# Optimization experiments

Measured on AMD Instinct MI355X. Metric: run time of the kernel, lower is better.

The kernel has to match this reference:

```python
import jax, jax.numpy as jnp
import numpy as np

HEADS = 24
HEAD_DIM = 128
EPS = 1e-6


def _rms_norm(x, w):
    # normalize over last dim (head_dim)
    var = jnp.mean(jnp.square(x), axis=-1, keepdims=True)
    return x * jax.lax.rsqrt(var + EPS) * w


def _rope_interleaved(x, cos, sin):
    # x: [B, S_img, H, D], cos/sin: [S_img, D//2]; non-neox (interleaved) style
    x1 = x[..., 0::2]
    x2 = x[..., 1::2]
    c = cos[None, :, None, :]
    s = sin[None, :, None, :]
    o1 = x1 * c - x2 * s
    o2 = x2 * c + x1 * s
    return jnp.stack([o1, o2], axis=-1).reshape(x.shape)


def setup_inputs() -> dict:
    key = jax.random.key(0)
    ks = jax.random.split(key, 5)
    B, S, D = 2, 2304, HEADS * HEAD_DIM
    S_img = 2048
    return {
        "hidden_states": jax.random.normal(ks[0], (B, S, D), dtype=jnp.float32),
        "w_qkv": jax.random.normal(ks[1], (3 * D, D), dtype=jnp.float32) * 0.02,
        "b_qkv": jax.random.normal(ks[2], (3 * D,), dtype=jnp.float32) * 0.02,
        "wq_norm": jnp.ones((HEAD_DIM,), dtype=jnp.float32),
        "wk_norm": jnp.ones((HEAD_DIM,), dtype=jnp.float32),
        "cos": jax.random.uniform(ks[3], (S_img, HEAD_DIM // 2), dtype=jnp.float32),
        "sin": jax.random.uniform(ks[4], (S_img, HEAD_DIM // 2), dtype=jnp.float32),
        "text_seq_len": 256,
    }


def reference(hidden_states, w_qkv, b_qkv, wq_norm, wk_norm, cos, sin, text_seq_len):
    B, S, D = hidden_states.shape
    T = text_seq_len
    # fused QKV projection
    qkv = hidden_states @ w_qkv.T + b_qkv  # [B, S, 3D]
    q, k, v = jnp.split(qkv, 3, axis=-1)
    q = q.reshape(B, S, HEADS, HEAD_DIM)
    k = k.reshape(B, S, HEADS, HEAD_DIM)
    v = v.reshape(B, S, HEADS, HEAD_DIM)
    # per-head RMSNorm on query/key
    q = _rms_norm(q, wq_norm)
    k = _rms_norm(k, wk_norm)
    # partial RoPE: only non-text (image/video) tokens
    q = jnp.concatenate([q[:, :T], _rope_interleaved(q[:, T:], cos, sin)], axis=1)
    k = jnp.concatenate([k[:, :T], _rope_interleaved(k[:, T:], cos, sin)], axis=1)
    # non-causal attention, scale = 1/sqrt(head_dim)
    scale = 1.0 / np.sqrt(HEAD_DIM).astype(np.float32)
    scores = jnp.einsum("bqhd,bkhd->bhqk", q, k) * scale
    probs = jax.nn.softmax(scores, axis=-1)
    out = jnp.einsum("bhqk,bkhd->bqhd", probs, v)
    return out.reshape(B, S, HEADS * HEAD_DIM)
```

## Files before the change

kernel.cpp:

```cpp
#include <hip/hip_runtime.h>
#include <stdint.h>
#include <stddef.h>

#define HEADS 24
#define HD    128
#define BB    2
#define SS    2304
#define DD    3072
#define NN3   9216
#define MM    4608

typedef unsigned short ushort_t;
typedef __bf16 bf16x8 __attribute__((ext_vector_type(8)));
typedef float  f32x4  __attribute__((ext_vector_type(4)));

union frag_u { bf16x8 f; uint4 v; unsigned d[4]; };

__device__ __forceinline__ unsigned short f2b(float f) {
  unsigned u = __float_as_uint(f);
  return (unsigned short)((u + 0x7fffu + ((u >> 16) & 1u)) >> 16);
}
__device__ __forceinline__ float b2f(unsigned short s) {
  return __uint_as_float(((unsigned)s) << 16);
}
__device__ __forceinline__ unsigned pkbf(float a, float b) {
  unsigned ua = (__float_as_uint(a) + 0x8000u) >> 16;
  unsigned ub = (__float_as_uint(b) + 0x8000u) & 0xffff0000u;
  return ua | ub;
}

__device__ __forceinline__ void gload_lds16(const void* g, void* l) {
#if __has_builtin(__builtin_amdgcn_global_load_lds)
  __builtin_amdgcn_global_load_lds(
      (const __attribute__((address_space(1))) unsigned int*)g,
      (__attribute__((address_space(3))) unsigned int*)l, 16, 0, 0);
#else
  *(uint4*)l = *(const uint4*)g;
#endif
}

__global__ __launch_bounds__(256) void cvt_bf16_kernel(
    const float* __restrict__ src, ushort_t* __restrict__ dst, int n8)
{
  int i = blockIdx.x * 256 + threadIdx.x;
  if (i >= n8) return;
  const float4* s = (const float4*)src + (size_t)i * 2;
  float4 a = s[0], b = s[1];
  union { ushort_t u[8]; uint4 v; } o;
  o.u[0] = f2b(a.x); o.u[1] = f2b(a.y); o.u[2] = f2b(a.z); o.u[3] = f2b(a.w);
  o.u[4] = f2b(b.x); o.u[5] = f2b(b.y); o.u[6] = f2b(b.z); o.u[7] = f2b(b.w);
  ((uint4*)dst)[i] = o.v;
}

#define BM 128
#define BN 128
#define BK 64
__global__ __launch_bounds__(256) void gemm_qkv_kernel(
    const ushort_t* __restrict__ A, const ushort_t* __restrict__ Bw,
    const float* __restrict__ bias, ushort_t* __restrict__ C)
{
  __shared__ ushort_t Al[BM * BK];
  __shared__ ushort_t Bl[BN * BK];
  const int t = threadIdx.x;
  const int w = t >> 6, l = t & 63;
  const int quad = l >> 4, lq = l & 15;
  const int wm = (w >> 1) << 6, wn = (w & 1) << 6;
  const int m0 = blockIdx.y * BM, n0 = blockIdx.x * BN;

  f32x4 acc[4][4] = {};

  for (int kb = 0; kb < DD; kb += BK) {
    __syncthreads();
#pragma unroll
    for (int i = 0; i < 4; ++i) {
      int c = i * 256 + t;
      int r = c >> 3, sub = c & 7;
      int gs = sub ^ (r & 7);
      gload_lds16(A + (size_t)(m0 + r) * DD + kb + gs * 8, (char*)Al + (size_t)c * 16);
      gload_lds16(Bw + (size_t)(n0 + r) * DD + kb + gs * 8, (char*)Bl + (size_t)c * 16);
    }
    __syncthreads();
#pragma unroll
    for (int ks = 0; ks < 2; ++ks) {
      bf16x8 af[4], bfr[4];
#pragma unroll
      for (int i = 0; i < 4; ++i) {
        int r = wm + i * 16 + lq;
        int ph = ((ks << 2) | quad) ^ (r & 7);
        af[i] = *(const bf16x8*)((const char*)Al + r * 128 + ph * 16);
      }
#pragma unroll
      for (int j = 0; j < 4; ++j) {
        int r = wn + j * 16 + lq;
        int ph = ((ks << 2) | quad) ^ (r & 7);
        bfr[j] = *(const bf16x8*)((const char*)Bl + r * 128 + ph * 16);
      }
#pragma unroll
      for (int i = 0; i < 4; ++i)
#pragma unroll
        for (int j = 0; j < 4; ++j)
          acc[i][j] = __builtin_amdgcn_mfma_f32_16x16x32_bf16(af[i], bfr[j], acc[i][j], 0, 0, 0);
    }
  }
#pragma unroll
  for (int j = 0; j < 4; ++j) {
    int n = n0 + wn + j * 16 + lq;
    float bj = bias[n];
#pragma unroll
    for (int i = 0; i < 4; ++i) {
      int mb = m0 + wm + i * 16 + quad * 4;
#pragma unroll
      for (int r = 0; r < 4; ++r)
        C[(size_t)(mb + r) * NN3 + n] = f2b(acc[i][j][r] + bj);
    }
  }
}

__global__ __launch_bounds__(256) void norm_rope_kernel(
    ushort_t* __restrict__ qkv, const float* __restrict__ wq,
    const float* __restrict__ wk, const float* __restrict__ cosb,
    const float* __restrict__ sinb, const int* __restrict__ tptr)
{
  const int T = *tptr;
  const int t = threadIdx.x, w = t >> 6, l = t & 63;
  int task = blockIdx.x * 4 + w;
  int which = task & 1;
  int rest = task >> 1;
  int h = rest % HEADS;
  int sm = rest / HEADS;
  int s = sm % SS;
  size_t base = (size_t)sm * NN3 + which * DD + h * HD + 2 * l;
  unsigned pr = *(const unsigned*)(qkv + base);
  float x1 = b2f((unsigned short)(pr & 0xffffu));
  float x2 = b2f((unsigned short)(pr >> 16));
  float ss = x1 * x1 + x2 * x2;
#pragma unroll
  for (int m = 1; m < 64; m <<= 1) ss += __shfl_xor(ss, m, 64);
  float rr = rsqrtf(ss * (1.0f / 128.0f) + 1e-6f);
  const float* wn = which ? wk : wq;
  float y1 = x1 * rr * wn[2 * l], y2 = x2 * rr * wn[2 * l + 1];
  if (s >= T) {
    float c = cosb[(size_t)(s - T) * 64 + l];
    float sn = sinb[(size_t)(s - T) * 64 + l];
    float o1 = y1 * c - y2 * sn;
    float o2 = y2 * c + y1 * sn;
    y1 = o1; y2 = o2;
  }
  *(unsigned*)(qkv + base) = (unsigned)f2b(y1) | ((unsigned)f2b(y2) << 16);
}

__global__ __launch_bounds__(256) void vtrans_kernel(
    const ushort_t* __restrict__ qkv, ushort_t* __restrict__ vt)
{
  __shared__ ushort_t Tl[HD * 73];
  const int t = threadIdx.x;
  const int st = blockIdx.x;
  const int bh = blockIdx.y;
  const int b = bh / HEADS, h = bh % HEADS;
  const int s0 = st * 64;
  const ushort_t* vsrc = qkv + (size_t)(b * SS) * NN3 + 2 * DD + h * HD;
#pragma unroll
  for (int i = 0; i < 4; ++i) {
    int c = i * 256 + t;
    int s = c >> 4, dc = c & 15;
    uint4 v4 = *(const uint4*)(vsrc + (size_t)(s0 + s) * NN3 + dc * 8);
    union { uint4 v; ushort_t u[8]; } un; un.v = v4;
#pragma unroll
    for (int j = 0; j < 8; ++j) Tl[(dc * 8 + j) * 73 + s] = un.u[j];
  }
  __syncthreads();
  ushort_t* vdst = vt + (size_t)bh * HD * SS;
#pragma unroll
  for (int i = 0; i < 4; ++i) {
    int c = i * 256 + t;
    int d = c >> 3, sc = c & 7;
    union { uint4 v; ushort_t u[8]; } un;
#pragma unroll
    for (int j = 0; j < 8; ++j) un.u[j] = Tl[d * 73 + sc * 8 + j];
    *(uint4*)(vdst + (size_t)d * SS + s0 + sc * 8) = un.v;
  }
}

__global__ __launch_bounds__(256, 2) void attn_kernel(
    const ushort_t* __restrict__ qkv, const ushort_t* __restrict__ vt,
    float* __restrict__ out)
{
  __shared__ char smem[65536];
  const int t = threadIdx.x;
  const int w = t >> 6, l = t & 63, quad = l >> 4, lq = l & 15;
  const int qt = blockIdx.x, bh = blockIdx.y;
  const int b = bh / HEADS, h = bh % HEADS;
  const int q0 = qt * 128;
  const ushort_t* qb = qkv + (size_t)(b * SS) * NN3 + h * HD;
  const ushort_t* Kg = qb + DD;
  const ushort_t* Vg = vt + (size_t)bh * HD * SS;

  frag_u aq[2][4];
#pragma unroll
  for (int m = 0; m < 2; ++m) {
    size_t ro = (size_t)(q0 + w * 32 + m * 16 + lq) * NN3;
#pragma unroll
    for (int kc = 0; kc < 4; ++kc)
      aq[m][kc].v = *(const uint4*)(qb + ro + kc * 32 + quad * 8);
  }

  frag_u ones;
  ones.d[0] = 0x3f803f80u; ones.d[1] = 0x3f803f80u;
  ones.d[2] = 0x3f803f80u; ones.d[3] = 0x3f803f80u;

  f32x4 o[2][8] = {};
  f32x4 lacc[2] = {};
  const float SC2 = 0.1275174315402f;
  const int rb = ((lq >> 2) << 3) | (lq & 3);

  {
#pragma unroll
    for (int i = 0; i < 4; ++i) {
      int n = i * 256 + t;
      int kv = n >> 4, c = n & 15;
      gload_lds16(Kg + (size_t)kv * NN3 + ((c ^ (kv & 15)) << 3), smem + n * 16);
    }
#pragma unroll
    for (int i = 0; i < 4; ++i) {
      int n = i * 256 + t;
      int dr = n >> 3, c = n & 7;
      gload_lds16(Vg + (size_t)dr * SS + ((c ^ (dr & 7)) << 3), smem + 32768 + n * 16);
    }
  }

  for (int kt = 0; kt < 36; ++kt) {
    char* Ksh = smem + (kt & 1) * 16384;
    char* Vsh = smem + 32768 + (kt & 1) * 16384;
    __syncthreads();
    if (kt + 1 < 36) {
      const int kv1 = (kt + 1) * 64;
      char* Kn = smem + ((kt + 1) & 1) * 16384;
      char* Vn = smem + 32768 + ((kt + 1) & 1) * 16384;
#pragma unroll
      for (int i = 0; i < 4; ++i) {
        int n = i * 256 + t;
        int kv = n >> 4, c = n & 15;
        gload_lds16(Kg + (size_t)(kv1 + kv) * NN3 + ((c ^ (kv & 15)) << 3), Kn + n * 16);
      }
#pragma unroll
      for (int i = 0; i < 4; ++i) {
        int n = i * 256 + t;
        int dr = n >> 3, c = n & 7;
        gload_lds16(Vg + (size_t)dr * SS + kv1 + ((c ^ (dr & 7)) << 3), Vn + n * 16);
      }
    }

    f32x4 sv[2][4] = {};
#pragma unroll
    for (int kc = 0; kc < 4; ++kc) {
#pragma unroll
      for (int kvb = 0; kvb < 4; ++kvb) {
        int row = ((kvb & 2) << 4) + ((kvb & 1) << 2) + rb;
        int swz = ((kc << 2) | quad) ^ (row & 15);
        frag_u a; a.v = *(const uint4*)(Ksh + row * 256 + swz * 16);
        sv[0][kvb] = __builtin_amdgcn_mfma_f32_16x16x32_bf16(a.f, aq[0][kc].f, sv[0][kvb], 0, 0, 0);
        sv[1][kvb] = __builtin_amdgcn_mfma_f32_16x16x32_bf16(a.f, aq[1][kc].f, sv[1][kvb], 0, 0, 0);
      }
    }

    uint2 pb[2][4];
#pragma unroll
    for (int m = 0; m < 2; ++m) {
#pragma unroll
      for (int kvb = 0; kvb < 4; ++kvb) {
        float p0 = exp2f(fmaf(sv[m][kvb][0], SC2, -8.0f));
        float p1 = exp2f(fmaf(sv[m][kvb][1], SC2, -8.0f));
        float p2 = exp2f(fmaf(sv[m][kvb][2], SC2, -8.0f));
        float p3 = exp2f(fmaf(sv[m][kvb][3], SC2, -8.0f));
        pb[m][kvb].x = pkbf(p0, p1);
        pb[m][kvb].y = pkbf(p2, p3);
      }
    }

#pragma unroll
    for (int kc2 = 0; kc2 < 2; ++kc2) {
      frag_u pf0, pf1;
      pf0.d[0] = pb[0][kc2 * 2].x;     pf0.d[1] = pb[0][kc2 * 2].y;
      pf0.d[2] = pb[0][kc2 * 2 + 1].x; pf0.d[3] = pb[0][kc2 * 2 + 1].y;
      pf1.d[0] = pb[1][kc2 * 2].x;     pf1.d[1] = pb[1][kc2 * 2].y;
      pf1.d[2] = pb[1][kc2 * 2 + 1].x; pf1.d[3] = pb[1][kc2 * 2 + 1].y;
      lacc[0] = __builtin_amdgcn_mfma_f32_16x16x32_bf16(ones.f, pf0.f, lacc[0], 0, 0, 0);
      lacc[1] = __builtin_amdgcn_mfma_f32_16x16x32_bf16(ones.f, pf1.f, lacc[1], 0, 0, 0);
#pragma unroll
      for (int dt = 0; dt < 8; ++dt) {
        int row = dt * 16 + lq;
        int swz = ((kc2 << 2) | quad) ^ (row & 7);
        frag_u a; a.v = *(const uint4*)(Vsh + row * 128 + swz * 16);
        o[0][dt] = __builtin_amdgcn_mfma_f32_16x16x32_bf16(a.f, pf0.f, o[0][dt], 0, 0, 0);
        o[1][dt] = __builtin_amdgcn_mfma_f32_16x16x32_bf16(a.f, pf1.f, o[1][dt], 0, 0, 0);
      }
    }
  }

  __syncthreads();
#pragma unroll
  for (int mch = 0; mch < 2; ++mch) {
    float inv = 1.0f / lacc[mch][0];
    int row = w * 16 + lq;
#pragma unroll
    for (int dt = 0; dt < 8; ++dt) {
      f32x4 val = o[mch][dt] * inv;
      int swz = ((dt << 2) | quad) ^ (row & 31);
      *(f32x4*)(smem + row * 512 + swz * 16) = val;
    }
    __syncthreads();
#pragma unroll
    for (int i = 0; i < 8; ++i) {
      int n = i * 256 + t;
      int rr = n >> 5, c = n & 31;
      f32x4 v = *(const f32x4*)(smem + rr * 512 + ((c ^ (rr & 31)) << 4));
      int qg = q0 + ((rr >> 4) << 5) + (mch << 4) + (rr & 15);
      *(f32x4*)(out + (size_t)(b * SS + qg) * DD + h * HD + c * 4) = v;
    }
    __syncthreads();
  }
}

extern "C" void kernel_launch(void* const* d_in, const int* in_sizes, int n_in,
                              void* d_out, int out_size, void* d_ws, size_t ws_size,
                              hipStream_t stream)
{
  const float* hs   = (const float*)d_in[0];
  const float* wqkv = (const float*)d_in[1];
  const float* bq   = (const float*)d_in[2];
  const float* wqn  = (const float*)d_in[3];
  const float* wkn  = (const float*)d_in[4];
  const float* cosb = (const float*)d_in[5];
  const float* sinb = (const float*)d_in[6];
  const int*   tseq = (const int*)d_in[7];
  float* out = (float*)d_out;
  char* ws = (char*)d_ws;

  ushort_t* hsb  = (ushort_t*)ws;
  ushort_t* wb   = (ushort_t*)(ws + 28311552);
  ushort_t* qkvb = (ushort_t*)(ws + 28311552 + 56623104);
  ushort_t* vtb  = hsb;

  cvt_bf16_kernel<<<6912, 256, 0, stream>>>(hs, hsb, 1769472);
  cvt_bf16_kernel<<<13824, 256, 0, stream>>>(wqkv, wb, 3538944);
  gemm_qkv_kernel<<<dim3(72, 36), 256, 0, stream>>>(hsb, wb, bq, qkvb);
  norm_rope_kernel<<<55296, 256, 0, stream>>>(qkvb, wqn, wkn, cosb, sinb, tseq);
  vtrans_kernel<<<dim3(36, 48), 256, 0, stream>>>(qkvb, vtb);
  attn_kernel<<<dim3(18, 48), 256, 0, stream>>>(qkvb, vtb, out);
}
```

Baseline: 796.4 us.

## Rewrite QKV GEMM as 256x256 tile, 8-wave, double-buffered pipelined kernel

Replaces the 128x128 single-buffered QKV GEMM with a 256x256-tile, 512-thread kernel. It double-buffers A/B tiles in 128KB LDS and interleaves global-to-LDS prefetch with MFMA quarter-phases using sched barriers, explicit waitcnts and s_setprio. It also swizzles the block order for L2 locality. The goal is to hide global memory latency and raise data reuse per tile. The trade-offs are far fewer blocks (648), heavy register use for 32 accumulators per lane, and fragile hand-scheduled synchronization.

```diff
diff --git a/kernel.cpp b/kernel.cpp
--- a/kernel.cpp
+++ b/kernel.cpp
@@ -39,6 +39,14 @@
 #endif
 }
 
+#define SCB() __builtin_amdgcn_sched_barrier(0)
+
+__device__ __forceinline__ void barx() {
+  asm volatile("" ::: "memory");
+  __builtin_amdgcn_s_barrier();
+  asm volatile("" ::: "memory");
+}
+
 __global__ __launch_bounds__(256) void cvt_bf16_kernel(
     const float* __restrict__ src, ushort_t* __restrict__ dst, int n8)
 {
@@ -52,63 +60,144 @@
   ((uint4*)dst)[i] = o.v;
 }
 
-#define BM 128
-#define BN 128
-#define BK 64
-__global__ __launch_bounds__(256) void gemm_qkv_kernel(
+#define NITER 24
+
+#define STG(Gp, rowbase, kt, ldsoff) do {                                          \
+    gload_lds16((Gp) + (size_t)((rowbase) + sr) * DD + (kt) * 64 + sgk,            \
+                smem + (ldsoff) + t * 16);                                         \
+    gload_lds16((Gp) + (size_t)((rowbase) + 64 + sr) * DD + (kt) * 64 + sgk,       \
+                smem + (ldsoff) + 8192 + t * 16);                                  \
+  } while (0)
+
+#define LOADA(base, mh) do {                                                       \
+    _Pragma("unroll") for (int ii = 0; ii < 4; ++ii) {                             \
+      int rl = (mh) * 64 + ii * 16 + lq;                                           \
+      _Pragma("unroll") for (int ks = 0; ks < 2; ++ks) {                           \
+        int ph = ((ks << 2) | quad) ^ (lq & 7);                                    \
+        af[ii][ks] = *(const bf16x8*)(smem + (base) + rl * 128 + ph * 16);         \
+      }                                                                            \
+    } } while (0)
+
+#define LOADB(base, nh) do {                                                       \
+    _Pragma("unroll") for (int jj = 0; jj < 2; ++jj) {                             \
+      int j = (nh) * 2 + jj;                                                       \
+      int rl = (wni & 1) * 64 + j * 16 + lq;                                       \
+      _Pragma("unroll") for (int ks = 0; ks < 2; ++ks) {                           \
+        int ph = ((ks << 2) | quad) ^ (lq & 7);                                    \
+        bfr[j][ks] = *(const bf16x8*)(smem + (base) + rl * 128 + ph * 16);         \
+      }                                                                            \
+    } } while (0)
+
+#define MFMAQ(mh, nh) do {                                                         \
+    _Pragma("unroll") for (int ii = 0; ii < 4; ++ii)                               \
+      _Pragma("unroll") for (int jj = 0; jj < 2; ++jj)                             \
+        _Pragma("unroll") for (int ks = 0; ks < 2; ++ks)                           \
+          acc[(mh) * 4 + ii][(nh) * 2 + jj] =                                      \
+              __builtin_amdgcn_mfma_f32_16x16x32_bf16(                             \
+                  af[ii][ks], bfr[(nh) * 2 + jj][ks],                              \
+                  acc[(mh) * 4 + ii][(nh) * 2 + jj], 0, 0, 0);                     \
+  } while (0)
+
+#define PH_MID() do {                                                              \
+    SCB(); barx(); SCB();                                                          \
+    asm volatile("s_waitcnt lgkmcnt(0)" ::: "memory");                             \
+    SCB();                                                                         \
+    __builtin_amdgcn_s_setprio(1);                                                 \
+  } while (0)
+
+#define PH_END() do {                                                              \
+    __builtin_amdgcn_s_setprio(0);                                                 \
+    SCB(); barx(); SCB();                                                          \
+  } while (0)
+
+#define PH_END_W(NWAIT) do {                                                       \
+    __builtin_amdgcn_s_setprio(0);                                                 \
+    SCB();                                                                         \
+    asm volatile("s_waitcnt vmcnt(" #NWAIT ")" ::: "memory");                      \
+    SCB(); barx(); SCB();                                                          \
+  } while (0)
+
+#define ONE_ITER(NL, TA) do {                                                      \
+    const int tb_ = (TA) + 1;                                                      \
+                                       \
+    LOADA(aoffA, 0); LOADB(boffA, 0);                                              \
+    STG(A, m0, tb_, 65536);                                                        \
+    PH_MID(); MFMAQ(0, 0); PH_END();                                               \
+                                       \
+    LOADB(boffA, 1);                                                               \
+    STG(A, m0 + 128, tb_, 65536 + 16384);                                          \
+    PH_MID(); MFMAQ(0, 1); PH_END();                                               \
+                                     \
+    LOADA(aoffA, 1);                                                               \
+    if (NL) STG(Bw, n0, (TA) + 2, 32768);                                          \
+    PH_MID(); MFMAQ(1, 1); PH_END();                                               \
+              \
+    if (NL) STG(Bw, n0 + 128, (TA) + 2, 49152);                                    \
+    PH_MID(); MFMAQ(1, 0);                                                         \
+    if (NL) { PH_END_W(4); } else { PH_END_W(0); }                                 \
+                                     \
+    LOADA(65536 + aoffA, 0); LOADB(65536 + boffA, 0);                              \
+    if (NL) STG(A, m0, (TA) + 2, 0);                                               \
+    PH_MID(); MFMAQ(0, 0); PH_END();                                               \
+                                     \
+    LOADB(65536 + boffA, 1);                                                       \
+    if (NL) STG(A, m0 + 128, (TA) + 2, 16384);                                     \
+    PH_MID(); MFMAQ(0, 1); PH_END();                                               \
+                                     \
+    LOADA(65536 + aoffA, 1);                                                       \
+    if (NL) STG(Bw, n0, tb_ + 2, 98304);                                           \
+    PH_MID(); MFMAQ(1, 1); PH_END();                                               \
+            \
+    if (NL) STG(Bw, n0 + 128, tb_ + 2, 114688);                                    \
+    PH_MID(); MFMAQ(1, 0);                                                         \
+    if (NL) { PH_END_W(4); } else { PH_END(); }                                    \
+  } while (0)
+
+__global__ __launch_bounds__(512, 2) void gemm_qkv_kernel(
     const ushort_t* __restrict__ A, const ushort_t* __restrict__ Bw,
     const float* __restrict__ bias, ushort_t* __restrict__ C)
 {
-  __shared__ ushort_t Al[BM * BK];
-  __shared__ ushort_t Bl[BN * BK];
+  __shared__ char smem[131072];
   const int t = threadIdx.x;
   const int w = t >> 6, l = t & 63;
   const int quad = l >> 4, lq = l & 15;
-  const int wm = (w >> 1) << 6, wn = (w & 1) << 6;
-  const int m0 = blockIdx.y * BM, n0 = blockIdx.x * BN;
-
-  f32x4 acc[4][4] = {};
-
-  for (int kb = 0; kb < DD; kb += BK) {
-    __syncthreads();
-#pragma unroll
-    for (int i = 0; i < 4; ++i) {
-      int c = i * 256 + t;
-      int r = c >> 3, sub = c & 7;
-      int gs = sub ^ (r & 7);
-      gload_lds16(A + (size_t)(m0 + r) * DD + kb + gs * 8, (char*)Al + (size_t)c * 16);
-      gload_lds16(Bw + (size_t)(n0 + r) * DD + kb + gs * 8, (char*)Bl + (size_t)c * 16);
-    }
-    __syncthreads();
-#pragma unroll
-    for (int ks = 0; ks < 2; ++ks) {
-      bf16x8 af[4], bfr[4];
-#pragma unroll
-      for (int i = 0; i < 4; ++i) {
-        int r = wm + i * 16 + lq;
-        int ph = ((ks << 2) | quad) ^ (r & 7);
-        af[i] = *(const bf16x8*)((const char*)Al + r * 128 + ph * 16);
-      }
-#pragma unroll
-      for (int j = 0; j < 4; ++j) {
-        int r = wn + j * 16 + lq;
-        int ph = ((ks << 2) | quad) ^ (r & 7);
-        bfr[j] = *(const bf16x8*)((const char*)Bl + r * 128 + ph * 16);
-      }
-#pragma unroll
-      for (int i = 0; i < 4; ++i)
-#pragma unroll
-        for (int j = 0; j < 4; ++j)
-          acc[i][j] = __builtin_amdgcn_mfma_f32_16x16x32_bf16(af[i], bfr[j], acc[i][j], 0, 0, 0);
-    }
-  }
+  const int wmi = w >> 2, wni = w & 3;
+
+  int orig = blockIdx.y * 36 + blockIdx.x;
+  int swz = (orig & 7) * 81 + (orig >> 3);
+  const int m0 = (swz / 36) * 256;
+  const int n0 = (swz % 36) * 256;
+
+  const int aoffA = wmi * 16384;
+  const int boffA = 32768 + (wni >> 1) * 16384;
+  const int sr = t >> 3, ssub = t & 7;
+  const int sgk = (ssub ^ (sr & 7)) << 3;
+
+  f32x4 acc[8][4] = {};
+  bf16x8 af[4][2], bfr[4][2];
+
+  STG(A,  m0,       0, 0);
+  STG(A,  m0 + 128, 0, 16384);
+  STG(Bw, n0,       0, 32768);
+  STG(Bw, n0 + 128, 0, 49152);
+  STG(Bw, n0,       1, 98304);
+  STG(Bw, n0 + 128, 1, 114688);
+  SCB();
+  asm volatile("s_waitcnt vmcnt(4)" ::: "memory");
+  SCB(); barx(); SCB();
+
+  for (int it = 0; it < NITER - 1; ++it) {
+    ONE_ITER(1, 2 * it);
+  }
+  ONE_ITER(0, 2 * (NITER - 1));
+
 #pragma unroll
   for (int j = 0; j < 4; ++j) {
-    int n = n0 + wn + j * 16 + lq;
+    int n = n0 + wni * 64 + j * 16 + lq;
     float bj = bias[n];
 #pragma unroll
-    for (int i = 0; i < 4; ++i) {
-      int mb = m0 + wm + i * 16 + quad * 4;
+    for (int i = 0; i < 8; ++i) {
+      int mb = m0 + wmi * 128 + i * 16 + quad * 4;
 #pragma unroll
       for (int r = 0; r < 4; ++r)
         C[(size_t)(mb + r) * NN3 + n] = f2b(acc[i][j][r] + bj);
@@ -343,7 +432,7 @@
 
   cvt_bf16_kernel<<<6912, 256, 0, stream>>>(hs, hsb, 1769472);
   cvt_bf16_kernel<<<13824, 256, 0, stream>>>(wqkv, wb, 3538944);
-  gemm_qkv_kernel<<<dim3(72, 36), 256, 0, stream>>>(hsb, wb, bq, qkvb);
+  gemm_qkv_kernel<<<dim3(36, 18), 512, 0, stream>>>(hsb, wb, bq, qkvb);
   norm_rope_kernel<<<55296, 256, 0, stream>>>(qkvb, wqn, wkn, cosb, sinb, tseq);
   vtrans_kernel<<<dim3(36, 48), 256, 0, stream>>>(qkvb, vtb);
   attn_kernel<<<dim3(18, 48), 256, 0, stream>>>(qkvb, vtb, out);
```

Result: faster. 721.8 us (-9.4%).
